# Optimization experiments

Measured on AMD Instinct MI355X. Metric: run time of the kernel, lower is better.

The kernel has to match this reference:

```python
import jax, jax.numpy as jnp
import numpy as np

K = 6
N_SAMPLES = 5
NOISE_FACTOR = 1.0
TEMP = 1.0
N_ITERS = 5
EPS = 1e-20
B = 131072
D_LAT = 16
D_FEAT = 8


def _sinkhorn(log_alpha):
    # iterative row/column logsumexp normalization on [M, K, K]
    for _ in range(N_ITERS):
        log_alpha = log_alpha - jax.scipy.special.logsumexp(log_alpha, axis=2, keepdims=True)
        log_alpha = log_alpha - jax.scipy.special.logsumexp(log_alpha, axis=1, keepdims=True)
    return jnp.exp(log_alpha)


def setup_inputs() -> dict:
    key = jax.random.key(0)
    ks = jax.random.split(key, 5)
    latent = jax.random.normal(ks[0], (B, D_LAT), dtype=jnp.float32)
    seq = jax.random.normal(ks[1], (B, K, D_FEAT), dtype=jnp.float32)
    noise_u = jax.random.uniform(ks[2], (N_SAMPLES * B, K, K), dtype=jnp.float32)
    W_sink = jax.random.normal(ks[3], (D_LAT, K * K), dtype=jnp.float32) * 0.1
    b_sink = jnp.zeros((K * K,), dtype=jnp.float32)
    W_mask = jax.random.normal(ks[4], (D_LAT, K), dtype=jnp.float32) * 0.1
    b_mask = jnp.zeros((K,), dtype=jnp.float32)
    return {"latent": latent, "seq": seq, "noise_u": noise_u,
            "W_sink": W_sink, "b_sink": b_sink, "W_mask": W_mask, "b_mask": b_mask}


def reference(latent, seq, noise_u, W_sink, b_sink, W_mask, b_mask):
    b = latent.shape[0]
    # sinknet: Linear(latent_dim, K*K) -> [B, K, K]
    log_alpha = (latent @ W_sink + b_sink).reshape(b, K, K)
    # gumbel_sinkhorn: tile over samples (sample-major, like torch .repeat)
    la = jnp.tile(log_alpha, (N_SAMPLES, 1, 1))  # [S*B, K, K]
    gumbel = -jnp.log(EPS - jnp.log(noise_u + EPS))
    la = (la + gumbel * NOISE_FACTOR) / TEMP
    sink = _sinkhorn(la)  # [S*B, K, K]
    # inv_soft_pers_flattened == transpose of each KxK matrix (same flat order)
    P = jnp.swapaxes(sink, 1, 2)
    seq_tiled = jnp.tile(seq, (N_SAMPLES, 1, 1))  # [S*B, K, D]
    ordered = jnp.matmul(P, seq_tiled)  # [S*B, K, D]
    # masknet: Linear + Softmax(dim=1)
    stopping = jax.nn.softmax(latent @ W_mask + b_mask, axis=1)  # [B, K]
    return ordered, stopping
```

## Files before the change

kernel.cpp:

```cpp
#include <hip/hip_runtime.h>

namespace {

constexpr int K     = 6;
constexpr int KK    = 36;
constexpr int DF    = 8;
constexpr int DLAT  = 16;
constexpr int NS    = 5;
constexpr int B     = 131072;
constexpr int M     = NS * B;
constexpr float EPS = 1e-20f;

__global__ __launch_bounds__(256) void fused_kernel(
    const float* __restrict__ latent,
    const float* __restrict__ seq,
    const float* __restrict__ noise,
    const float* __restrict__ W_sink,
    const float* __restrict__ b_sink,
    const float* __restrict__ W_mask,
    const float* __restrict__ b_mask,
    float* __restrict__ out,
    float* __restrict__ stopping)
{
    const int b = blockIdx.x * 256 + threadIdx.x;

    float lat[DLAT];
    const float4* lat4 = reinterpret_cast<const float4*>(latent + (size_t)b * DLAT);
    #pragma unroll
    for (int k = 0; k < 4; ++k) {
        float4 v = lat4[k];
        lat[k*4+0] = v.x; lat[k*4+1] = v.y; lat[k*4+2] = v.z; lat[k*4+3] = v.w;
    }

    float ela[KK];
    #pragma unroll
    for (int i = 0; i < KK; ++i) ela[i] = b_sink[i];
    #pragma unroll
    for (int k = 0; k < DLAT; ++k) {
        const float lv = lat[k];
        #pragma unroll
        for (int i = 0; i < KK; ++i)
            ela[i] = fmaf(lv, W_sink[k*KK + i], ela[i]);
    }

    {
        float v[K];
        #pragma unroll
        for (int i = 0; i < K; ++i) v[i] = b_mask[i];
        #pragma unroll
        for (int k = 0; k < DLAT; ++k) {
            const float lv = lat[k];
            #pragma unroll
            for (int i = 0; i < K; ++i)
                v[i] = fmaf(lv, W_mask[k*K + i], v[i]);
        }
        float mx = v[0];
        #pragma unroll
        for (int i = 1; i < K; ++i) mx = fmaxf(mx, v[i]);
        float sum = 0.f;
        #pragma unroll
        for (int i = 0; i < K; ++i) { v[i] = __expf(v[i] - mx); sum += v[i]; }
        const float inv = __builtin_amdgcn_rcpf(sum);
        float2* o2 = reinterpret_cast<float2*>(stopping + (size_t)b * K);
        o2[0] = make_float2(v[0]*inv, v[1]*inv);
        o2[1] = make_float2(v[2]*inv, v[3]*inv);
        o2[2] = make_float2(v[4]*inv, v[5]*inv);
    }

    #pragma unroll
    for (int i = 0; i < KK; ++i) ela[i] = __expf(ela[i]);

    float sq[K*DF];
    const float4* s4 = reinterpret_cast<const float4*>(seq + (size_t)b * (K*DF));
    #pragma unroll
    for (int q = 0; q < 12; ++q) {
        float4 v = s4[q];
        sq[q*4+0] = v.x; sq[q*4+1] = v.y; sq[q*4+2] = v.z; sq[q*4+3] = v.w;
    }

    #pragma unroll
    for (int s = 0; s < NS; ++s) {
        const size_t row = (size_t)s * B + b;

        float p[KK];
        {
            const float4* n4 = reinterpret_cast<const float4*>(noise + row * KK);
            #pragma unroll
            for (int q = 0; q < 9; ++q) {
                float4 u = n4[q];
                p[q*4+0] = ela[q*4+0] * __builtin_amdgcn_rcpf(EPS - __logf(u.x + EPS));
                p[q*4+1] = ela[q*4+1] * __builtin_amdgcn_rcpf(EPS - __logf(u.y + EPS));
                p[q*4+2] = ela[q*4+2] * __builtin_amdgcn_rcpf(EPS - __logf(u.z + EPS));
                p[q*4+3] = ela[q*4+3] * __builtin_amdgcn_rcpf(EPS - __logf(u.w + EPS));
            }
        }

        #pragma unroll
        for (int it = 0; it < 5; ++it) {
            #pragma unroll
            for (int i = 0; i < K; ++i) {
                const float sum = ((p[i*K+0] + p[i*K+1]) + (p[i*K+2] + p[i*K+3]))
                                + (p[i*K+4] + p[i*K+5]);
                const float r = __builtin_amdgcn_rcpf(sum);
                #pragma unroll
                for (int j = 0; j < K; ++j) p[i*K+j] *= r;
            }
            #pragma unroll
            for (int j = 0; j < K; ++j) {
                const float sum = ((p[0*K+j] + p[1*K+j]) + (p[2*K+j] + p[3*K+j]))
                                + (p[4*K+j] + p[5*K+j]);
                const float r = __builtin_amdgcn_rcpf(sum);
                #pragma unroll
                for (int i = 0; i < K; ++i) p[i*K+j] *= r;
            }
        }

        float4* o4 = reinterpret_cast<float4*>(out + row * (K*DF));
        #pragma unroll
        for (int i = 0; i < K; ++i) {
            float orow[DF];
            #pragma unroll
            for (int d = 0; d < DF; ++d) orow[d] = 0.f;
            #pragma unroll
            for (int j = 0; j < K; ++j) {
                const float pv = p[j*K + i];
                #pragma unroll
                for (int d = 0; d < DF; ++d)
                    orow[d] = fmaf(pv, sq[j*DF + d], orow[d]);
            }
            float4 v0, v1;
            v0.x = orow[0]; v0.y = orow[1]; v0.z = orow[2]; v0.w = orow[3];
            v1.x = orow[4]; v1.y = orow[5]; v1.z = orow[6]; v1.w = orow[7];
            o4[i*2 + 0] = v0;
            o4[i*2 + 1] = v1;
        }
    }
}

}

extern "C" void kernel_launch(void* const* d_in, const int* in_sizes, int n_in,
                              void* d_out, int out_size, void* d_ws, size_t ws_size,
                              hipStream_t stream) {
    const float* latent = (const float*)d_in[0];
    const float* seq    = (const float*)d_in[1];
    const float* noise  = (const float*)d_in[2];
    const float* W_sink = (const float*)d_in[3];
    const float* b_sink = (const float*)d_in[4];
    const float* W_mask = (const float*)d_in[5];
    const float* b_mask = (const float*)d_in[6];
    float* out      = (float*)d_out;
    float* stopping = out + (size_t)M * K * DF;

    fused_kernel<<<B / 256, 256, 0, stream>>>(latent, seq, noise,
                                              W_sink, b_sink, W_mask, b_mask,
                                              out, stopping);
}
```

Measured before the change: 94.55 us.

## Split samples across blocks and stage noise loads through LDS for coalescing

Each block now handles one sample and 256 batch rows, so the grid grows fivefold and the per-thread serial loop over samples is gone. Noise is read with coalesced nontemporal wave-wide loads, then transposed through shared memory so each thread gets its own 36 values. Outputs are written with nontemporal stores, and the stopping softmax runs only in sample-0 blocks. The cost is that the latent projection and exp are recomputed in every sample block and seq is re-read five times, plus extra LDS traffic and a launch_bounds occupancy hint.

```diff
diff --git a/kernel.cpp b/kernel.cpp
--- a/kernel.cpp
+++ b/kernel.cpp
@@ -11,7 +11,9 @@
 constexpr int M     = NS * B;
 constexpr float EPS = 1e-20f;
 
-__global__ __launch_bounds__(256) void fused_kernel(
+typedef float f32x4 __attribute__((ext_vector_type(4)));
+
+__global__ __launch_bounds__(256, 4) void fused_kernel(
     const float* __restrict__ latent,
     const float* __restrict__ seq,
     const float* __restrict__ noise,
@@ -22,37 +24,55 @@
     float* __restrict__ out,
     float* __restrict__ stopping)
 {
-    const int b = blockIdx.x * 256 + threadIdx.x;
+    __shared__ f32x4 nbuf[4][64 * 9];
+
+    const int bid = blockIdx.x;
+    const int s   = bid % NS;
+    const int bc  = bid / NS;
+    const int t   = threadIdx.x;
+    const int w   = t >> 6;
+    const int l   = t & 63;
+    const int b   = bc * 256 + t;
+    const size_t row = (size_t)s * B + b;
+
+    const f32x4* nsrc = reinterpret_cast<const f32x4*>(noise)
+                      + ((size_t)s * B + (size_t)bc * 256 + (size_t)w * 64) * 9;
+    f32x4 stage[9];
+    #pragma unroll
+    for (int j = 0; j < 9; ++j)
+        stage[j] = __builtin_nontemporal_load(&nsrc[l + 64 * j]);
 
     float lat[DLAT];
-    const float4* lat4 = reinterpret_cast<const float4*>(latent + (size_t)b * DLAT);
-    #pragma unroll
-    for (int k = 0; k < 4; ++k) {
-        float4 v = lat4[k];
-        lat[k*4+0] = v.x; lat[k*4+1] = v.y; lat[k*4+2] = v.z; lat[k*4+3] = v.w;
+    {
+        const float4* lat4 = reinterpret_cast<const float4*>(latent + (size_t)b * DLAT);
+        #pragma unroll
+        for (int k2 = 0; k2 < 4; ++k2) {
+            float4 v = lat4[k2];
+            lat[k2*4+0] = v.x; lat[k2*4+1] = v.y; lat[k2*4+2] = v.z; lat[k2*4+3] = v.w;
+        }
     }
 
     float ela[KK];
     #pragma unroll
     for (int i = 0; i < KK; ++i) ela[i] = b_sink[i];
     #pragma unroll
-    for (int k = 0; k < DLAT; ++k) {
-        const float lv = lat[k];
+    for (int k2 = 0; k2 < DLAT; ++k2) {
+        const float lv = lat[k2];
         #pragma unroll
         for (int i = 0; i < KK; ++i)
-            ela[i] = fmaf(lv, W_sink[k*KK + i], ela[i]);
+            ela[i] = fmaf(lv, W_sink[k2*KK + i], ela[i]);
     }
 
-    {
+    if (s == 0) {
         float v[K];
         #pragma unroll
         for (int i = 0; i < K; ++i) v[i] = b_mask[i];
         #pragma unroll
-        for (int k = 0; k < DLAT; ++k) {
-            const float lv = lat[k];
+        for (int k2 = 0; k2 < DLAT; ++k2) {
+            const float lv = lat[k2];
             #pragma unroll
             for (int i = 0; i < K; ++i)
-                v[i] = fmaf(lv, W_mask[k*K + i], v[i]);
+                v[i] = fmaf(lv, W_mask[k2*K + i], v[i]);
         }
         float mx = v[0];
         #pragma unroll
@@ -70,70 +90,70 @@
     #pragma unroll
     for (int i = 0; i < KK; ++i) ela[i] = __expf(ela[i]);
 
-    float sq[K*DF];
-    const float4* s4 = reinterpret_cast<const float4*>(seq + (size_t)b * (K*DF));
     #pragma unroll
-    for (int q = 0; q < 12; ++q) {
-        float4 v = s4[q];
-        sq[q*4+0] = v.x; sq[q*4+1] = v.y; sq[q*4+2] = v.z; sq[q*4+3] = v.w;
+    for (int j = 0; j < 9; ++j)
+        nbuf[w][l + 64 * j] = stage[j];
+    asm volatile("" ::: "memory");
+    f32x4 nr[9];
+    #pragma unroll
+    for (int j = 0; j < 9; ++j)
+        nr[j] = nbuf[w][l * 9 + j];
+
+    float p[KK];
+    #pragma unroll
+    for (int j = 0; j < 9; ++j) {
+        f32x4 u = nr[j];
+        p[j*4+0] = ela[j*4+0] * __builtin_amdgcn_rcpf(EPS - __logf(u.x + EPS));
+        p[j*4+1] = ela[j*4+1] * __builtin_amdgcn_rcpf(EPS - __logf(u.y + EPS));
+        p[j*4+2] = ela[j*4+2] * __builtin_amdgcn_rcpf(EPS - __logf(u.z + EPS));
+        p[j*4+3] = ela[j*4+3] * __builtin_amdgcn_rcpf(EPS - __logf(u.w + EPS));
     }
 
     #pragma unroll
-    for (int s = 0; s < NS; ++s) {
-        const size_t row = (size_t)s * B + b;
-
-        float p[KK];
-        {
-            const float4* n4 = reinterpret_cast<const float4*>(noise + row * KK);
-            #pragma unroll
-            for (int q = 0; q < 9; ++q) {
-                float4 u = n4[q];
-                p[q*4+0] = ela[q*4+0] * __builtin_amdgcn_rcpf(EPS - __logf(u.x + EPS));
-                p[q*4+1] = ela[q*4+1] * __builtin_amdgcn_rcpf(EPS - __logf(u.y + EPS));
-                p[q*4+2] = ela[q*4+2] * __builtin_amdgcn_rcpf(EPS - __logf(u.z + EPS));
-                p[q*4+3] = ela[q*4+3] * __builtin_amdgcn_rcpf(EPS - __logf(u.w + EPS));
-            }
-        }
-
-        #pragma unroll
-        for (int it = 0; it < 5; ++it) {
-            #pragma unroll
-            for (int i = 0; i < K; ++i) {
-                const float sum = ((p[i*K+0] + p[i*K+1]) + (p[i*K+2] + p[i*K+3]))
-                                + (p[i*K+4] + p[i*K+5]);
-                const float r = __builtin_amdgcn_rcpf(sum);
-                #pragma unroll
-                for (int j = 0; j < K; ++j) p[i*K+j] *= r;
-            }
-            #pragma unroll
-            for (int j = 0; j < K; ++j) {
-                const float sum = ((p[0*K+j] + p[1*K+j]) + (p[2*K+j] + p[3*K+j]))
-                                + (p[4*K+j] + p[5*K+j]);
-                const float r = __builtin_amdgcn_rcpf(sum);
-                #pragma unroll
-                for (int i = 0; i < K; ++i) p[i*K+j] *= r;
-            }
-        }
-
-        float4* o4 = reinterpret_cast<float4*>(out + row * (K*DF));
+    for (int it = 0; it < 5; ++it) {
         #pragma unroll
         for (int i = 0; i < K; ++i) {
-            float orow[DF];
+            const float sum = ((p[i*K+0] + p[i*K+1]) + (p[i*K+2] + p[i*K+3]))
+                            + (p[i*K+4] + p[i*K+5]);
+            const float r = __builtin_amdgcn_rcpf(sum);
             #pragma unroll
-            for (int d = 0; d < DF; ++d) orow[d] = 0.f;
+            for (int j = 0; j < K; ++j) p[i*K+j] *= r;
+        }
+        #pragma unroll
+        for (int j = 0; j < K; ++j) {
+            const float sum = ((p[0*K+j] + p[1*K+j]) + (p[2*K+j] + p[3*K+j]))
+                            + (p[4*K+j] + p[5*K+j]);
+            const float r = __builtin_amdgcn_rcpf(sum);
             #pragma unroll
-            for (int j = 0; j < K; ++j) {
-                const float pv = p[j*K + i];
-                #pragma unroll
-                for (int d = 0; d < DF; ++d)
-                    orow[d] = fmaf(pv, sq[j*DF + d], orow[d]);
-            }
-            float4 v0, v1;
-            v0.x = orow[0]; v0.y = orow[1]; v0.z = orow[2]; v0.w = orow[3];
-            v1.x = orow[4]; v1.y = orow[5]; v1.z = orow[6]; v1.w = orow[7];
-            o4[i*2 + 0] = v0;
-            o4[i*2 + 1] = v1;
+            for (int i = 0; i < K; ++i) p[i*K+j] *= r;
         }
+    }
+
+    float o[K*DF];
+    #pragma unroll
+    for (int i = 0; i < K*DF; ++i) o[i] = 0.f;
+
+    const float4* s4 = reinterpret_cast<const float4*>(seq + (size_t)b * (K*DF));
+    #pragma unroll
+    for (int j = 0; j < K; ++j) {
+        float4 a0 = s4[j*2 + 0];
+        float4 a1 = s4[j*2 + 1];
+        float srow[DF] = {a0.x, a0.y, a0.z, a0.w, a1.x, a1.y, a1.z, a1.w};
+        #pragma unroll
+        for (int i = 0; i < K; ++i) {
+            const float pv = p[j*K + i];
+            #pragma unroll
+            for (int d = 0; d < DF; ++d)
+                o[i*DF + d] = fmaf(pv, srow[d], o[i*DF + d]);
+        }
+    }
+
+    f32x4* o4 = reinterpret_cast<f32x4*>(out + row * (K*DF));
+    #pragma unroll
+    for (int q = 0; q < 12; ++q) {
+        f32x4 v;
+        v.x = o[q*4+0]; v.y = o[q*4+1]; v.z = o[q*4+2]; v.w = o[q*4+3];
+        __builtin_nontemporal_store(v, &o4[q]);
     }
 }
 
@@ -152,7 +172,7 @@
     float* out      = (float*)d_out;
     float* stopping = out + (size_t)M * K * DF;
 
-    fused_kernel<<<B / 256, 256, 0, stream>>>(latent, seq, noise,
+    fused_kernel<<<M / 256, 256, 0, stream>>>(latent, seq, noise,
                                               W_sink, b_sink, W_mask, b_mask,
                                               out, stopping);
 }
```

After: 324.5 us. 3.43x slower.
